# Performance work log

Measured on AMD Instinct MI355X. Metric: run time of the kernel, lower is better.

The kernel has to match this reference:

```python
import jax, jax.numpy as jnp
import numpy as np

B, CLN, QL, IH, IW = 64, 32, 32, 16, 16
CDF, SL = 256, 128
IDF = CLN * IH * IW  # 8192


def setup_inputs() -> dict:
    key = jax.random.key(0)
    k1, k2, k3 = jax.random.split(key, 3)
    inp = jax.random.normal(k1, (B, CLN, QL, IH, IW), dtype=jnp.float32)
    context = jax.random.normal(k2, (B, CDF, SL), dtype=jnp.float32)
    # Conv2d(cdf, idf, 1, bias=False) weight, squeezed to [idf, cdf]
    W = jax.random.normal(k3, (IDF, CDF), dtype=jnp.float32) * (1.0 / np.sqrt(CDF))
    return {"input": inp, "context": context, "W": W}


def reference(input, context, W):
    b, cln, queryL, ih, iw = input.shape
    idf = cln * ih * iw
    sourceL = context.shape[2]
    # target: b x queryL x (cln*ih*iw)
    targetT = jnp.transpose(input, (0, 2, 1, 3, 4)).reshape(b, queryL, idf)
    # 1x1 conv projection of context: b x idf x sourceL
    sourceT = jnp.einsum('oc,bcs->bos', W, context)
    # attention scores and softmax over sourceL (nn.Softmax on 2D -> dim=1)
    attn = jnp.einsum('bqd,bds->bqs', targetT, sourceT)  # b x queryL x sourceL
    attn = jax.nn.softmax(attn, axis=-1)
    attnT = jnp.transpose(attn, (0, 2, 1))  # b x sourceL x queryL
    # weighted context: b x idf x queryL
    wc = jnp.einsum('bds,bsq->bdq', sourceT, attnT)
    # faithful to torch .view: raw row-major reinterpretation of [b, idf, queryL]
    wc = wc.reshape(b, queryL, cln, ih, iw)
    wc = jnp.transpose(wc, (0, 2, 1, 3, 4))  # b x cln x queryL x ih x iw
    return (wc, attnT)
```

## Files before the change

kernel.cpp:

```cpp
#include <hip/hip_runtime.h>
#include <math.h>


#define ZK 16

typedef _Float16 f16x8 __attribute__((ext_vector_type(8)));
typedef float f32x4 __attribute__((ext_vector_type(4)));

#define GLDS16(gp, lp)                                                          \
    __builtin_amdgcn_global_load_lds(                                           \
        (const __attribute__((address_space(1))) void*)(gp),                    \
        (__attribute__((address_space(3))) void*)(lp), 16, 0, 0)

__global__ __launch_bounds__(256) void k0a_prep(const float* __restrict__ Wm,
                                                _Float16* __restrict__ Wth,
                                                _Float16* __restrict__ Wtl) {
    const int kb = blockIdx.x;
    const int t = threadIdx.x;
    __shared__ float tile[32][260];
    {
        const int r = t >> 3;
        const int c0 = (t & 7) * 32;
        const float* src = Wm + (long)(kb * 32 + r) * 256 + c0;
#pragma unroll
        for (int i = 0; i < 8; ++i) {
            float4 v = *(const float4*)(src + i * 4);
            tile[r][c0 + i * 4 + 0] = v.x;
            tile[r][c0 + i * 4 + 1] = v.y;
            tile[r][c0 + i * 4 + 2] = v.z;
            tile[r][c0 + i * 4 + 3] = v.w;
        }
    }
    __syncthreads();
    const int lane = t & 63;
    const int quad = lane >> 4, l15 = lane & 15;
#pragma unroll
    for (int i = 0; i < 4; ++i) {
        int nsub = (t >> 6) * 4 + i;
        f16x8 oh, ol;
#pragma unroll
        for (int j = 0; j < 8; ++j) {
            float f = tile[quad * 8 + j][nsub * 16 + l15];
            _Float16 h = (_Float16)f;
            oh[j] = h;
            ol[j] = (_Float16)(f - (float)h);
        }
        long addr = ((long)(kb * 16 + nsub) * 64 + lane) * 8;
        *(f16x8*)(Wth + addr) = oh;
        *(f16x8*)(Wtl + addr) = ol;
    }
}

__global__ __launch_bounds__(256) void k0b_prep(const float* __restrict__ Wm,
                                                _Float16* __restrict__ Wbf) {
    const int t = threadIdx.x;
    const int fid = blockIdx.x * 4 + (t >> 6);
    const int mb = fid >> 3, kb4 = fid & 7;
    const int lane = t & 63;
    const int quad = lane >> 4, l15 = lane & 15;
    const float* src = Wm + (long)(mb * 16 + l15) * 256 + kb4 * 32 + quad * 8;
    float4 u0 = *(const float4*)(src);
    float4 u1 = *(const float4*)(src + 4);
    f16x8 o;
    o[0] = (_Float16)u0.x; o[1] = (_Float16)u0.y;
    o[2] = (_Float16)u0.z; o[3] = (_Float16)u0.w;
    o[4] = (_Float16)u1.x; o[5] = (_Float16)u1.y;
    o[6] = (_Float16)u1.z; o[7] = (_Float16)u1.w;
    *(f16x8*)(Wbf + ((long)fid * 64 + lane) * 8) = o;
}

__global__ __launch_bounds__(512, 2) void k1_mfma(const float* __restrict__ inp,
                                                  const _Float16* __restrict__ Wth,
                                                  const _Float16* __restrict__ Wtl,
                                                  float* __restrict__ tWpart) {
    const int lin = blockIdx.x + (blockIdx.y << 4);
    const int kz = lin & 15;
    const int m0 = (lin >> 4) * 128;
    const int t = threadIdx.x;
    const int lane = t & 63, wv = t >> 6;
    const int quad = lane >> 4, l15 = lane & 15;
    const int mi = wv >> 2;
    const int ni = wv & 3;

    __shared__ float As[3][128][32];

    const int srow = t >> 3;
    const int swc = ((t & 7) ^ (srow & 7)) * 4;
    const float* sb0;
    const float* sb1;
    {
        int mA = m0 + srow;
        sb0 = inp + (long)(mA >> 5) * 262144 + (long)(mA & 31) * 256 + swc;
        mA = m0 + 64 + srow;
        sb1 = inp + (long)(mA >> 5) * 262144 + (long)(mA & 31) * 256 + swc;
    }

    f32x4 acc[4][4];
#pragma unroll
    for (int i = 0; i < 4; ++i)
#pragma unroll
        for (int j = 0; j < 4; ++j) acc[i][j] = (f32x4){0.f, 0.f, 0.f, 0.f};

    f16x8 Bh[2][4], Bl[2][4];

    {
        long o = (long)((kz * 512) >> 8) * 8192 + ((kz * 512) & 255);
        GLDS16(sb0 + o, &As[0][0][0] + wv * 256);
        GLDS16(sb1 + o, &As[0][64][0] + wv * 256);
        const int k1g = kz * 512 + 32;
        o = (long)(k1g >> 8) * 8192 + (k1g & 255);
        GLDS16(sb0 + o, &As[1][0][0] + wv * 256);
        GLDS16(sb1 + o, &As[1][64][0] + wv * 256);
        const long bb = ((long)((kz * 16) * 16 + ni * 4) * 64 + lane) * 8;
#pragma unroll
        for (int j = 0; j < 4; ++j) {
            Bh[0][j] = *(const f16x8*)(Wth + bb + (long)j * 512);
            Bl[0][j] = *(const f16x8*)(Wtl + bb + (long)j * 512);
        }
    }

#pragma unroll
    for (int it = 0; it < 16; ++it) {
        const int cur = it & 1, nxt = cur ^ 1;
        if (it < 15) asm volatile("s_waitcnt vmcnt(10)" ::: "memory");
        else         asm volatile("s_waitcnt vmcnt(0)" ::: "memory");
        __builtin_amdgcn_sched_barrier(0);
        __builtin_amdgcn_s_barrier();
        __builtin_amdgcn_sched_barrier(0);

        if (it < 14) {
            const int kg = kz * 512 + (it + 2) * 32;
            const long o = (long)(kg >> 8) * 8192 + (kg & 255);
            GLDS16(sb0 + o, &As[(it + 2) % 3][0][0] + wv * 256);
            GLDS16(sb1 + o, &As[(it + 2) % 3][64][0] + wv * 256);
        }
        if (it < 15) {
            const long bb = ((long)((kz * 16 + it + 1) * 16 + ni * 4) * 64 + lane) * 8;
#pragma unroll
            for (int j = 0; j < 4; ++j) {
                Bh[nxt][j] = *(const f16x8*)(Wth + bb + (long)j * 512);
                Bl[nxt][j] = *(const f16x8*)(Wtl + bb + (long)j * 512);
            }
        }
        __builtin_amdgcn_sched_barrier(0);

        f16x8 ah[4], al[4];
#pragma unroll
        for (int i = 0; i < 4; ++i) {
            const int row = (mi * 4 + i) * 16 + l15;
            const int x = row & 7;
            float4 f0 = *(const float4*)&As[it % 3][row][((quad * 2) ^ x) * 4];
            float4 f1 = *(const float4*)&As[it % 3][row][((quad * 2 + 1) ^ x) * 4];
            float ff[8] = {f0.x, f0.y, f0.z, f0.w, f1.x, f1.y, f1.z, f1.w};
#pragma unroll
            for (int j = 0; j < 8; ++j) {
                _Float16 h = (_Float16)ff[j];
                ah[i][j] = h;
                al[i][j] = (_Float16)(ff[j] - (float)h);
            }
        }

#pragma unroll
        for (int i = 0; i < 4; ++i)
#pragma unroll
            for (int j = 0; j < 4; ++j) {
                acc[i][j] = __builtin_amdgcn_mfma_f32_16x16x32_f16(ah[i], Bh[cur][j], acc[i][j], 0, 0, 0);
                acc[i][j] = __builtin_amdgcn_mfma_f32_16x16x32_f16(al[i], Bh[cur][j], acc[i][j], 0, 0, 0);
                acc[i][j] = __builtin_amdgcn_mfma_f32_16x16x32_f16(ah[i], Bl[cur][j], acc[i][j], 0, 0, 0);
            }
    }

    float* outp = tWpart + (long)kz * 524288;
#pragma unroll
    for (int i = 0; i < 4; ++i) {
        const int mbase = m0 + (mi * 4 + i) * 16 + quad * 4;
#pragma unroll
        for (int j = 0; j < 4; ++j) {
            const int c = (ni * 4 + j) * 16 + l15;
#pragma unroll
            for (int rg = 0; rg < 4; ++rg)
                outp[(long)(mbase + rg) * 256 + c] = acc[i][j][rg];
        }
    }
}

__global__ __launch_bounds__(256) void k2_logits_softmax(const float* __restrict__ tWpart,
                                                         const float* __restrict__ ctx,
                                                         float* __restrict__ attnT) {
    const int qg = blockIdx.x;
    const int b  = blockIdx.y;
    const int t  = threadIdx.x;
    __shared__ float tw4[4][256];
#pragma unroll
    for (int qq = 0; qq < 4; ++qq) {
        const float* p = tWpart + (long)(b * 32 + qg * 4 + qq) * 256 + t;
        float s = 0.f;
#pragma unroll
        for (int z = 0; z < ZK; ++z) s += p[(long)z * 524288];
        tw4[qq][t] = s;
    }
    __syncthreads();
    const int q = t >> 6, lane = t & 63;
    const float* ctxb = ctx + (long)b * 32768 + lane * 2;
    float ax = 0.f, ay = 0.f;
#pragma unroll 4
    for (int c = 0; c < 256; ++c) {
        float tw = tw4[q][c];
        float2 cv = *(const float2*)(ctxb + c * 128);
        ax = fmaf(tw, cv.x, ax);
        ay = fmaf(tw, cv.y, ay);
    }
    float mx = fmaxf(ax, ay);
#pragma unroll
    for (int m = 1; m <= 32; m <<= 1) mx = fmaxf(mx, __shfl_xor(mx, m));
    float ex = expf(ax - mx);
    float ey = expf(ay - mx);
    float sm = ex + ey;
#pragma unroll
    for (int m = 1; m <= 32; m <<= 1) sm += __shfl_xor(sm, m);
    float inv = 1.f / sm;
    ex *= inv; ey *= inv;
    float* o = attnT + (long)b * 4096 + (qg * 4 + q);
    o[(lane * 2 + 0) * 32] = ex;
    o[(lane * 2 + 1) * 32] = ey;
}

__global__ __launch_bounds__(256) void k3_ctxA(const float* __restrict__ ctx,
                                               const float* __restrict__ attnT,
                                               _Float16* __restrict__ ctxAqf) {
    const int cg = blockIdx.x;
    const int b  = blockIdx.y;
    const int t  = threadIdx.x;
    __shared__ float at[128][32];
    __shared__ float cs[32][132];
#pragma unroll
    for (int i = 0; i < 4; ++i)
        *(float4*)((float*)at + i * 1024 + t * 4) =
            *(const float4*)(attnT + (long)b * 4096 + i * 1024 + t * 4);
#pragma unroll
    for (int i = 0; i < 4; ++i) {
        int idx = i * 256 + t;
        int c = idx >> 5, sseg = (idx & 31) * 4;
        *(float4*)&cs[c][sseg] = *(const float4*)(ctx + (long)b * 32768 + (long)(cg * 32 + c) * 128 + sseg);
    }
    __syncthreads();
    const int c = t >> 3;
    const int qs = (t & 7) * 4;
    float4 acc = make_float4(0.f, 0.f, 0.f, 0.f);
#pragma unroll 4
    for (int s = 0; s < 128; ++s) {
        float cv = cs[c][s];
        float4 av = *(const float4*)&at[s][qs];
        acc.x = fmaf(cv, av.x, acc.x);
        acc.y = fmaf(cv, av.y, acc.y);
        acc.z = fmaf(cv, av.z, acc.z);
        acc.w = fmaf(cv, av.w, acc.w);
    }
    const int cglob = cg * 32 + c;
    const long cpart = (long)(cglob >> 5) * 64 + 16 * ((cglob >> 3) & 3);
    float vals[4] = {acc.x, acc.y, acc.z, acc.w};
#pragma unroll
    for (int u = 0; u < 4; ++u) {
        int n = b * 32 + qs + u;
        long addr = ((long)(n >> 4) * 8 * 64 + cpart + (n & 15)) * 8 + (cglob & 7);
        ctxAqf[addr] = (_Float16)vals[u];
    }
}

__global__ __launch_bounds__(256) void k4_mfma(const _Float16* __restrict__ Wbf,
                                               const _Float16* __restrict__ ctxAqf,
                                               float* __restrict__ out0) {
    const int t = threadIdx.x;
    const int lane = t & 63, wv = t >> 6;
    const int mb = blockIdx.x * 4 + wv;
    const int nb0 = blockIdx.y * 8;

    __shared__ _Float16 Bs[32768];

    {
        const _Float16* gsrc = ctxAqf + (long)nb0 * 4096;
#pragma unroll
        for (int i = 0; i < 16; ++i) {
            const int chunk = i * 256 + wv * 64;
            GLDS16(gsrc + (long)chunk * 8 + lane * 8, Bs + chunk * 8);
        }
    }
    __syncthreads();

    const _Float16* abase = Wbf + ((long)mb * 8 * 64 + lane) * 8;

    f32x4 acc[8];
#pragma unroll
    for (int j = 0; j < 8; ++j) acc[j] = (f32x4){0.f, 0.f, 0.f, 0.f};

#pragma unroll
    for (int kb = 0; kb < 8; ++kb) {
        f16x8 af = *(const f16x8*)(abase + (long)kb * 512);
#pragma unroll
        for (int j = 0; j < 8; ++j) {
            f16x8 bf = *(const f16x8*)(Bs + (j * 8 + kb) * 512 + lane * 8);
            acc[j] = __builtin_amdgcn_mfma_f32_16x16x32_f16(af, bf, acc[j], 0, 0, 0);
        }
    }
    const int quad = lane >> 4, col = lane & 15;
#pragma unroll
    for (int j = 0; j < 8; ++j) {
        const int n = (nb0 + j) * 16 + col;
        float* ob = out0 + (long)(n >> 5) * 262144 + (n & 31);
#pragma unroll
        for (int rg = 0; rg < 4; ++rg) {
            const int d = mb * 16 + quad * 4 + rg;
            ob[(long)((d >> 3) & 31) * 8192 + (long)(d >> 8) * 256 + (long)(d & 7) * 32] = acc[j][rg];
        }
    }
}

extern "C" void kernel_launch(void* const* d_in, const int* in_sizes, int n_in,
                              void* d_out, int out_size, void* d_ws, size_t ws_size,
                              hipStream_t stream) {
    const float* inp = (const float*)d_in[0];
    const float* ctx = (const float*)d_in[1];
    const float* Wm  = (const float*)d_in[2];
    float* out0 = (float*)d_out;
    float* out1 = out0 + 16777216;

    float* wsf = (float*)d_ws;
    float* tWpart = wsf;
    _Float16* Wbf    = (_Float16*)wsf;
    _Float16* ctxAqf = (_Float16*)(wsf + 1048576);
    _Float16* Wth = (_Float16*)(wsf + 8388608);
    _Float16* Wtl = Wth + 2097152;

    hipLaunchKernelGGL(k0a_prep, dim3(256), dim3(256), 0, stream, Wm, Wth, Wtl);
    hipLaunchKernelGGL(k1_mfma, dim3(16, ZK), dim3(512), 0, stream, inp, Wth, Wtl, tWpart);
    hipLaunchKernelGGL(k2_logits_softmax, dim3(8, 64), dim3(256), 0, stream, tWpart, ctx, out1);
    hipLaunchKernelGGL(k0b_prep, dim3(1024), dim3(256), 0, stream, Wm, Wbf);
    hipLaunchKernelGGL(k3_ctxA, dim3(8, 64), dim3(256), 0, stream, ctx, out1, ctxAqf);
    hipLaunchKernelGGL(k4_mfma, dim3(128, 16), dim3(256), 0, stream, Wbf, ctxAqf, out0);
}
```

Measured before the change: 218.2 us.

## Split A to fp16 hi/lo once per element in LDS, shrink k1 tile

Restructures k1 so each thread loads its A slice from global into registers, converts it once to packed fp16 hi/lo pairs with cvt_pkrtz, and stores those into LDS in fragment order. Before, the fp32 tile was staged in LDS and every wave redundantly converted its own fragments. The block shrinks from 512 to 256 threads with a 64-row M tile, the grid doubles, and the MFMA issue is regrouped into three passes. Costs: a register-prefetch double buffer replaces the async global-to-LDS triple buffer, each iteration now needs an LDS write plus a barrier, and B-fragment reuse per block is lower.

```diff
diff --git a/kernel.cpp b/kernel.cpp
--- a/kernel.cpp
+++ b/kernel.cpp
@@ -5,6 +5,7 @@
 #define ZK 16
 
 typedef _Float16 f16x8 __attribute__((ext_vector_type(8)));
+typedef __fp16 h16x2 __attribute__((ext_vector_type(2)));
 typedef float f32x4 __attribute__((ext_vector_type(4)));
 
 #define GLDS16(gp, lp)                                                          \
@@ -69,31 +70,26 @@
     *(f16x8*)(Wbf + ((long)fid * 64 + lane) * 8) = o;
 }
 
-__global__ __launch_bounds__(512, 2) void k1_mfma(const float* __restrict__ inp,
+__global__ __launch_bounds__(256, 2) void k1_mfma(const float* __restrict__ inp,
                                                   const _Float16* __restrict__ Wth,
                                                   const _Float16* __restrict__ Wtl,
                                                   float* __restrict__ tWpart) {
-    const int lin = blockIdx.x + (blockIdx.y << 4);
-    const int kz = lin & 15;
-    const int m0 = (lin >> 4) * 128;
+    const int kz = blockIdx.x;
+    const int m0 = blockIdx.y * 64;
     const int t = threadIdx.x;
     const int lane = t & 63, wv = t >> 6;
     const int quad = lane >> 4, l15 = lane & 15;
-    const int mi = wv >> 2;
-    const int ni = wv & 3;
-
-    __shared__ float As[3][128][32];
-
-    const int srow = t >> 3;
-    const int swc = ((t & 7) ^ (srow & 7)) * 4;
-    const float* sb0;
-    const float* sb1;
+
+    __shared__ _Float16 Fh[2][4][64][8];
+    __shared__ _Float16 Fl[2][4][64][8];
+
+    const float* arow;
     {
-        int mA = m0 + srow;
-        sb0 = inp + (long)(mA >> 5) * 262144 + (long)(mA & 31) * 256 + swc;
-        mA = m0 + 64 + srow;
-        sb1 = inp + (long)(mA >> 5) * 262144 + (long)(mA & 31) * 256 + swc;
-    }
+        const int mA = m0 + (t >> 2);
+        arow = inp + (long)(mA >> 5) * 262144 + (long)(mA & 31) * 256 + (t & 3) * 8;
+    }
+    _Float16* wh = &Fh[0][t >> 6][((t & 3) << 4) | ((t >> 2) & 15)][0];
+    _Float16* wl = &Fl[0][t >> 6][((t & 3) << 4) | ((t >> 2) & 15)][0];
 
     f32x4 acc[4][4];
 #pragma unroll
@@ -101,17 +97,15 @@
 #pragma unroll
         for (int j = 0; j < 4; ++j) acc[i][j] = (f32x4){0.f, 0.f, 0.f, 0.f};
 
+    float4 Ar[2][2];
     f16x8 Bh[2][4], Bl[2][4];
 
     {
-        long o = (long)((kz * 512) >> 8) * 8192 + ((kz * 512) & 255);
-        GLDS16(sb0 + o, &As[0][0][0] + wv * 256);
-        GLDS16(sb1 + o, &As[0][64][0] + wv * 256);
-        const int k1g = kz * 512 + 32;
-        o = (long)(k1g >> 8) * 8192 + (k1g & 255);
-        GLDS16(sb0 + o, &As[1][0][0] + wv * 256);
-        GLDS16(sb1 + o, &As[1][64][0] + wv * 256);
-        const long bb = ((long)((kz * 16) * 16 + ni * 4) * 64 + lane) * 8;
+        const int kg = kz * 512;
+        const long off = (long)(kg >> 8) * 8192 + (kg & 255);
+        Ar[0][0] = *(const float4*)(arow + off);
+        Ar[0][1] = *(const float4*)(arow + off + 4);
+        const long bb = ((long)((kz * 16) * 16 + wv * 4) * 64 + lane) * 8;
 #pragma unroll
         for (int j = 0; j < 4; ++j) {
             Bh[0][j] = *(const f16x8*)(Wth + bb + (long)j * 512);
@@ -122,20 +116,12 @@
 #pragma unroll
     for (int it = 0; it < 16; ++it) {
         const int cur = it & 1, nxt = cur ^ 1;
-        if (it < 15) asm volatile("s_waitcnt vmcnt(10)" ::: "memory");
-        else         asm volatile("s_waitcnt vmcnt(0)" ::: "memory");
-        __builtin_amdgcn_sched_barrier(0);
-        __builtin_amdgcn_s_barrier();
-        __builtin_amdgcn_sched_barrier(0);
-
-        if (it < 14) {
-            const int kg = kz * 512 + (it + 2) * 32;
-            const long o = (long)(kg >> 8) * 8192 + (kg & 255);
-            GLDS16(sb0 + o, &As[(it + 2) % 3][0][0] + wv * 256);
-            GLDS16(sb1 + o, &As[(it + 2) % 3][64][0] + wv * 256);
-        }
         if (it < 15) {
-            const long bb = ((long)((kz * 16 + it + 1) * 16 + ni * 4) * 64 + lane) * 8;
+            const int kg = kz * 512 + (it + 1) * 32;
+            const long off = (long)(kg >> 8) * 8192 + (kg & 255);
+            Ar[nxt][0] = *(const float4*)(arow + off);
+            Ar[nxt][1] = *(const float4*)(arow + off + 4);
+            const long bb = ((long)((kz * 16 + it + 1) * 16 + wv * 4) * 64 + lane) * 8;
 #pragma unroll
             for (int j = 0; j < 4; ++j) {
                 Bh[nxt][j] = *(const f16x8*)(Wth + bb + (long)j * 512);
@@ -144,39 +130,57 @@
         }
         __builtin_amdgcn_sched_barrier(0);
 
+        {
+            const float4 a0 = Ar[cur][0], a1 = Ar[cur][1];
+            h16x2 h01 = __builtin_amdgcn_cvt_pkrtz(a0.x, a0.y);
+            h16x2 h23 = __builtin_amdgcn_cvt_pkrtz(a0.z, a0.w);
+            h16x2 h45 = __builtin_amdgcn_cvt_pkrtz(a1.x, a1.y);
+            h16x2 h67 = __builtin_amdgcn_cvt_pkrtz(a1.z, a1.w);
+            h16x2 l01 = __builtin_amdgcn_cvt_pkrtz(a0.x - (float)h01[0], a0.y - (float)h01[1]);
+            h16x2 l23 = __builtin_amdgcn_cvt_pkrtz(a0.z - (float)h23[0], a0.w - (float)h23[1]);
+            h16x2 l45 = __builtin_amdgcn_cvt_pkrtz(a1.x - (float)h45[0], a1.y - (float)h45[1]);
+            h16x2 l67 = __builtin_amdgcn_cvt_pkrtz(a1.z - (float)h67[0], a1.w - (float)h67[1]);
+            union { f16x8 v; h16x2 p[4]; } H, L;
+            H.p[0] = h01; H.p[1] = h23; H.p[2] = h45; H.p[3] = h67;
+            L.p[0] = l01; L.p[1] = l23; L.p[2] = l45; L.p[3] = l67;
+            *(f16x8*)(wh + cur * 2048) = H.v;
+            *(f16x8*)(wl + cur * 2048) = L.v;
+        }
+        asm volatile("s_waitcnt lgkmcnt(0)" ::: "memory");
+        __builtin_amdgcn_sched_barrier(0);
+        __builtin_amdgcn_s_barrier();
+        __builtin_amdgcn_sched_barrier(0);
+
         f16x8 ah[4], al[4];
 #pragma unroll
         for (int i = 0; i < 4; ++i) {
-            const int row = (mi * 4 + i) * 16 + l15;
-            const int x = row & 7;
-            float4 f0 = *(const float4*)&As[it % 3][row][((quad * 2) ^ x) * 4];
-            float4 f1 = *(const float4*)&As[it % 3][row][((quad * 2 + 1) ^ x) * 4];
-            float ff[8] = {f0.x, f0.y, f0.z, f0.w, f1.x, f1.y, f1.z, f1.w};
-#pragma unroll
-            for (int j = 0; j < 8; ++j) {
-                _Float16 h = (_Float16)ff[j];
-                ah[i][j] = h;
-                al[i][j] = (_Float16)(ff[j] - (float)h);
-            }
-        }
-
+            ah[i] = *(const f16x8*)&Fh[cur][i][lane][0];
+            al[i] = *(const f16x8*)&Fl[cur][i][lane][0];
+        }
 #pragma unroll
         for (int i = 0; i < 4; ++i)
 #pragma unroll
-            for (int j = 0; j < 4; ++j) {
+            for (int j = 0; j < 4; ++j)
                 acc[i][j] = __builtin_amdgcn_mfma_f32_16x16x32_f16(ah[i], Bh[cur][j], acc[i][j], 0, 0, 0);
+#pragma unroll
+        for (int i = 0; i < 4; ++i)
+#pragma unroll
+            for (int j = 0; j < 4; ++j)
                 acc[i][j] = __builtin_amdgcn_mfma_f32_16x16x32_f16(al[i], Bh[cur][j], acc[i][j], 0, 0, 0);
+#pragma unroll
+        for (int i = 0; i < 4; ++i)
+#pragma unroll
+            for (int j = 0; j < 4; ++j)
                 acc[i][j] = __builtin_amdgcn_mfma_f32_16x16x32_f16(ah[i], Bl[cur][j], acc[i][j], 0, 0, 0);
-            }
     }
 
     float* outp = tWpart + (long)kz * 524288;
 #pragma unroll
     for (int i = 0; i < 4; ++i) {
-        const int mbase = m0 + (mi * 4 + i) * 16 + quad * 4;
+        const int mbase = m0 + i * 16 + quad * 4;
 #pragma unroll
         for (int j = 0; j < 4; ++j) {
-            const int c = (ni * 4 + j) * 16 + l15;
+            const int c = (wv * 4 + j) * 16 + l15;
 #pragma unroll
             for (int rg = 0; rg < 4; ++rg)
                 outp[(long)(mbase + rg) * 256 + c] = acc[i][j][rg];
@@ -332,7 +336,7 @@
     _Float16* Wtl = Wth + 2097152;
 
     hipLaunchKernelGGL(k0a_prep, dim3(256), dim3(256), 0, stream, Wm, Wth, Wtl);
-    hipLaunchKernelGGL(k1_mfma, dim3(16, ZK), dim3(512), 0, stream, inp, Wth, Wtl, tWpart);
+    hipLaunchKernelGGL(k1_mfma, dim3(16, 32), dim3(256), 0, stream, inp, Wth, Wtl, tWpart);
     hipLaunchKernelGGL(k2_logits_softmax, dim3(8, 64), dim3(256), 0, stream, tWpart, ctx, out1);
     hipLaunchKernelGGL(k0b_prep, dim3(1024), dim3(256), 0, stream, Wm, Wbf);
     hipLaunchKernelGGL(k3_ctxA, dim3(8, 64), dim3(256), 0, stream, ctx, out1, ctxAqf);
```

Result: faster. 207.3 us (-5.0%).
